# Optimization experiments

Measured on AMD Instinct MI355X. Metric: run time of the kernel, lower is better.

## Reference

```python
import jax, jax.numpy as jnp
import numpy as np

B, N, OBS, ACT = 4, 256, 40, 8
HEAD, DIM = 8, 32
T = HEAD * DIM


def setup_inputs() -> dict:
    key = jax.random.key(0)
    ks = jax.random.split(key, 10)
    x = jax.random.normal(ks[0], (B, N + 1, OBS), dtype=jnp.float32)
    # last row, col 0 carries the (float-encoded) target intersection index
    tgt = jax.random.randint(ks[1], (B,), 0, N)
    x = x.at[:, -1, 0].set(tgt.astype(jnp.float32))
    adj = jax.random.uniform(ks[2], (N, N), dtype=jnp.float32)
    s = 0.02
    return {
        "x": x,
        "adj": adj,
        "We1": jax.random.normal(ks[3], (OBS, T), dtype=jnp.float32) * s,
        "be1": jnp.zeros((T,), jnp.float32),
        "We2": jax.random.normal(ks[4], (T, T), dtype=jnp.float32) * s,
        "be2": jnp.zeros((T,), jnp.float32),
        "Wl": jax.random.normal(ks[5], (T, T), dtype=jnp.float32) * s,
        "bl": jnp.zeros((T,), jnp.float32),
        "Wn": jax.random.normal(ks[6], (T, T), dtype=jnp.float32) * s,
        "bn": jnp.zeros((T,), jnp.float32),
        "Wh": jax.random.normal(ks[7], (T, T), dtype=jnp.float32) * s,
        "bh": jnp.zeros((T,), jnp.float32),
        "Wa": jax.random.normal(ks[8], (DIM, ACT), dtype=jnp.float32) * s,
        "ba": jnp.zeros((ACT,), jnp.float32),
    }


def reference(x, adj, We1, be1, We2, be2, Wl, bl, Wn, bn, Wh, bh, Wa, ba):
    b, np1, _ = x.shape
    n = np1 - 1
    tgt = x[:, -1, 0].astype(jnp.int32)          # [B] target intersection ids
    obs = x[:, :-1, :]                            # [B,N,OBS]
    # obs_embed: Linear+ReLU twice
    emb = jax.nn.relu(obs @ We1 + be1)
    emb = jax.nn.relu(emb @ We2 + be2)            # [B,N,T]
    # tile then matmul by adjacency: result is adj @ emb, replicated along dim 1
    ne = jnp.einsum('mn,bnd->bmd', adj, emb)      # [B,N,T]
    ne = jnp.broadcast_to(ne[:, None], (b, n, n, T))  # [B,N,N,T] (tiled, as in torch)
    # agent heads: [B,N,H,1,D]
    ah = jax.nn.relu(emb @ Wl + bl).reshape(b, n, 1, DIM, HEAD).transpose(0, 1, 4, 2, 3)
    # neighbor heads: [B,N,H,N,D]
    nh = jax.nn.relu(ne @ Wn + bn).reshape(b, n, n, DIM, HEAD).transpose(0, 1, 4, 2, 3)
    # einsum 'ijklm,ijknm->ijklm' with l=1: elementwise over d, summed over n
    attn = ah * nh.sum(axis=3, keepdims=True)     # [B,N,H,1,D]
    attn = jax.nn.softmax(attn, axis=-1)
    hid = jax.nn.relu(ne @ Wh + bh).reshape(b, n, n, DIM, HEAD).transpose(0, 1, 4, 2, 3)
    out = attn * hid.sum(axis=3, keepdims=True)   # [B,N,H,1,D]
    out = out.mean(axis=2).reshape(b, n, DIM)     # mean over heads -> [B,N,D]
    g = out[jnp.arange(b), tgt]                   # gather per-batch target row [B,D]
    act = g @ Wa + ba                             # [B,ACT]
    return act
```

## Files before the change

### kernel.cpp

```cpp
#include <hip/hip_runtime.h>

#define Bsz 4
#define Nn  256
#define OBSD 40
#define ACTD 8
#define HEADS 8
#define DIMD 32
#define Td  256
#define R   4

#define FMA4(accr, s, wv) \
    (accr).x = fmaf((s), (wv).x, (accr).x); \
    (accr).y = fmaf((s), (wv).y, (accr).y); \
    (accr).z = fmaf((s), (wv).z, (accr).z); \
    (accr).w = fmaf((s), (wv).w, (accr).w)

__global__ __launch_bounds__(512, 1) void k_emb(
                      const float* __restrict__ x,
                      const float* __restrict__ We1, const float* __restrict__ be1,
                      const float* __restrict__ We2, const float* __restrict__ be2,
                      float* __restrict__ emb,
                      float* __restrict__ snh, float* __restrict__ shid) {
    int g = blockIdx.x;
    int t = threadIdx.x;
    int row0 = g * R;
    int b = row0 >> 8;
    int n0 = row0 & 255;
    if (g == 0)      { for (int i = t; i < Bsz * Td; i += 512) snh[i]  = 0.f; }
    else if (g == 1) { for (int i = t; i < Bsz * Td; i += 512) shid[i] = 0.f; }

    __shared__ float4 obs_t[OBSD];
    __shared__ float4 h1_t[Td];
    __shared__ float4 part[8][R][64];
    if (t < R * OBSD) {
        int r = t & (R - 1), k = t >> 2;
        ((float*)&obs_t[k])[r] = x[(b * (Nn + 1) + n0 + r) * OBSD + k];
    }
    __syncthreads();

    if (t < Td) {
        float bias1 = be1[t];
        float a1[R] = {bias1, bias1, bias1, bias1};
        float wbuf[8];
#pragma unroll
        for (int p = 0; p < 8; ++p) wbuf[p] = We1[p * Td + t];
#pragma unroll
        for (int k = 0; k < OBSD; ++k) {
            float w = wbuf[k & 7];
            if (k + 8 < OBSD) wbuf[k & 7] = We1[(k + 8) * Td + t];
            float4 ov = obs_t[k];
            a1[0] = fmaf(ov.x, w, a1[0]);
            a1[1] = fmaf(ov.y, w, a1[1]);
            a1[2] = fmaf(ov.z, w, a1[2]);
            a1[3] = fmaf(ov.w, w, a1[3]);
        }
        h1_t[t] = make_float4(fmaxf(a1[0], 0.f), fmaxf(a1[1], 0.f),
                              fmaxf(a1[2], 0.f), fmaxf(a1[3], 0.f));
    }
    __syncthreads();

    int wv = t >> 6, c = t & 63;
    {
        float4 a2[R] = {};
        float4 buf[8];
#pragma unroll
        for (int p = 0; p < 8; ++p)
            buf[p] = *(const float4*)(We2 + ((wv << 5) + p) * Td + 4 * c);
#pragma unroll
        for (int i = 0; i < 32; ++i) {
            int k = (wv << 5) + i;
            float4 wvv = buf[i & 7];
            if (i + 8 < 32)
                buf[i & 7] = *(const float4*)(We2 + (k + 8) * Td + 4 * c);
            float4 hv = h1_t[k];
            FMA4(a2[0], hv.x, wvv);
            FMA4(a2[1], hv.y, wvv);
            FMA4(a2[2], hv.z, wvv);
            FMA4(a2[3], hv.w, wvv);
        }
#pragma unroll
        for (int r = 0; r < R; ++r) part[wv][r][c] = a2[r];
    }
    __syncthreads();

    if (t < Td) {
        int c2 = t >> 2, j = t & 3;
#pragma unroll
        for (int r = 0; r < R; ++r) {
            float v = be2[t];
#pragma unroll
            for (int w2 = 0; w2 < 8; ++w2) v += ((const float*)&part[w2][r][c2])[j];
            emb[(row0 + r) * Td + t] = fmaxf(v, 0.f);
        }
    }
}

__global__ __launch_bounds__(512, 1) void k_fused(
                        const float* __restrict__ adj, const float* __restrict__ emb,
                        const float* __restrict__ Wn, const float* __restrict__ bn,
                        const float* __restrict__ Wh, const float* __restrict__ bh,
                        float* __restrict__ snh, float* __restrict__ shid) {
    int g = blockIdx.x, b = blockIdx.y;
    int t = threadIdx.x;
    int m0 = g * R;
    __shared__ float4 arow_t[Nn];
    __shared__ float4 nrow_t[Td];
    __shared__ float4 partN[8][R][64];
    __shared__ float4 partH[8][R][64];
    if (t < Td)
        arow_t[t] = make_float4(adj[(m0 + 0) * Nn + t], adj[(m0 + 1) * Nn + t],
                                adj[(m0 + 2) * Nn + t], adj[(m0 + 3) * Nn + t]);
    __syncthreads();

    int wv = t >> 6, c = t & 63;
    const float* eb = emb + b * Nn * Td;

    {
        float4 aN[R] = {};
        float4 buf[8];
#pragma unroll
        for (int p = 0; p < 8; ++p)
            buf[p] = *(const float4*)(eb + ((wv << 5) + p) * Td + 4 * c);
#pragma unroll
        for (int i = 0; i < 32; ++i) {
            int n = (wv << 5) + i;
            float4 ev = buf[i & 7];
            if (i + 8 < 32)
                buf[i & 7] = *(const float4*)(eb + (n + 8) * Td + 4 * c);
            float4 ar = arow_t[n];
            FMA4(aN[0], ar.x, ev);
            FMA4(aN[1], ar.y, ev);
            FMA4(aN[2], ar.z, ev);
            FMA4(aN[3], ar.w, ev);
        }
#pragma unroll
        for (int r = 0; r < R; ++r) partN[wv][r][c] = aN[r];
    }
    __syncthreads();
    if (t < Td) {
        int c2 = t >> 2, j = t & 3;
        float nr[R];
#pragma unroll
        for (int r = 0; r < R; ++r) {
            float v = 0.f;
#pragma unroll
            for (int w2 = 0; w2 < 8; ++w2) v += ((const float*)&partN[w2][r][c2])[j];
            nr[r] = v;
        }
        nrow_t[t] = make_float4(nr[0], nr[1], nr[2], nr[3]);
    }
    __syncthreads();

    {
        float4 sN[R] = {};
        float4 sH[R] = {};
        float4 bufN[4], bufH[4];
#pragma unroll
        for (int p = 0; p < 4; ++p) {
            int k = (wv << 5) + p;
            bufN[p] = *(const float4*)(Wn + k * Td + 4 * c);
            bufH[p] = *(const float4*)(Wh + k * Td + 4 * c);
        }
#pragma unroll
        for (int i = 0; i < 32; ++i) {
            int k = (wv << 5) + i;
            float4 wn4 = bufN[i & 3];
            float4 wh4 = bufH[i & 3];
            if (i + 4 < 32) {
                bufN[i & 3] = *(const float4*)(Wn + (k + 4) * Td + 4 * c);
                bufH[i & 3] = *(const float4*)(Wh + (k + 4) * Td + 4 * c);
            }
            float4 nv = nrow_t[k];
            FMA4(sN[0], nv.x, wn4);  FMA4(sH[0], nv.x, wh4);
            FMA4(sN[1], nv.y, wn4);  FMA4(sH[1], nv.y, wh4);
            FMA4(sN[2], nv.z, wn4);  FMA4(sH[2], nv.z, wh4);
            FMA4(sN[3], nv.w, wn4);  FMA4(sH[3], nv.w, wh4);
        }
#pragma unroll
        for (int r = 0; r < R; ++r) { partN[wv][r][c] = sN[r]; partH[wv][r][c] = sH[r]; }
    }
    __syncthreads();

    if (t < Td) {
        int c2 = t >> 2, j = t & 3;
        float bnt = bn[t], bht = bh[t];
        float rs1 = 0.f, rs2 = 0.f;
#pragma unroll
        for (int r = 0; r < R; ++r) {
            float v1 = bnt, v2 = bht;
#pragma unroll
            for (int w2 = 0; w2 < 8; ++w2) {
                v1 += ((const float*)&partN[w2][r][c2])[j];
                v2 += ((const float*)&partH[w2][r][c2])[j];
            }
            rs1 += fmaxf(v1, 0.f);
            rs2 += fmaxf(v2, 0.f);
        }
        atomicAdd(&snh[b * Td + t], rs1);
        atomicAdd(&shid[b * Td + t], rs2);
    }
}

__global__ __launch_bounds__(256, 1) void k_final(
                        const float* __restrict__ x, const float* __restrict__ emb,
                        const float* __restrict__ Wl, const float* __restrict__ bl,
                        const float* __restrict__ snh, const float* __restrict__ shid,
                        const float* __restrict__ Wa, const float* __restrict__ ba,
                        float* __restrict__ out) {
    int b = blockIdx.x;
    int t = threadIdx.x;
    int tgt = (int)x[(b * (Nn + 1) + Nn) * OBSD + 0];
    tgt = tgt < 0 ? 0 : (tgt > Nn - 1 ? Nn - 1 : tgt);
    __shared__ float erow[Td], lg[Td], p[Td], od[DIMD];
    __shared__ float4 partL[4][64];
    erow[t] = emb[(b * Nn + tgt) * Td + t];
    __syncthreads();

    int wv = t >> 6, c = t & 63;
    {
        float4 aL = {};
        float4 buf[8];
#pragma unroll
        for (int pp = 0; pp < 8; ++pp)
            buf[pp] = *(const float4*)(Wl + ((wv << 6) + pp) * Td + 4 * c);
#pragma unroll
        for (int i = 0; i < 64; ++i) {
            int k = (wv << 6) + i;
            float4 wlv = buf[i & 7];
            if (i + 8 < 64)
                buf[i & 7] = *(const float4*)(Wl + (k + 8) * Td + 4 * c);
            FMA4(aL, erow[k], wlv);
        }
        partL[wv][c] = aL;
    }
    __syncthreads();

    int c2 = t >> 2, j = t & 3;
    float acc = bl[t];
#pragma unroll
    for (int w2 = 0; w2 < 4; ++w2) acc += ((const float*)&partL[w2][c2])[j];
    float ah = fmaxf(acc, 0.f);
    lg[t] = ah * snh[b * Td + t];
    __syncthreads();
    int h = t & 7;
    float mx = -1e30f;
#pragma unroll
    for (int d = 0; d < DIMD; ++d) mx = fmaxf(mx, lg[d * HEADS + h]);
    float se = 0.f;
#pragma unroll
    for (int d = 0; d < DIMD; ++d) se += __expf(lg[d * HEADS + h] - mx);
    float attn = __expf(lg[t] - mx) / se;
    p[t] = attn * shid[b * Td + t];
    __syncthreads();
    if (t < DIMD) {
        float s = 0.f;
#pragma unroll
        for (int hh = 0; hh < HEADS; ++hh) s += p[t * HEADS + hh];
        od[t] = s * (1.f / HEADS);
    }
    __syncthreads();
    if (t < ACTD) {
        float s = ba[t];
#pragma unroll
        for (int d = 0; d < DIMD; ++d) s = fmaf(od[d], Wa[d * ACTD + t], s);
        out[b * ACTD + t] = s;
    }
}

extern "C" void kernel_launch(void* const* d_in, const int* in_sizes, int n_in,
                              void* d_out, int out_size, void* d_ws, size_t ws_size,
                              hipStream_t stream) {
    const float* x   = (const float*)d_in[0];
    const float* adj = (const float*)d_in[1];
    const float* We1 = (const float*)d_in[2];
    const float* be1 = (const float*)d_in[3];
    const float* We2 = (const float*)d_in[4];
    const float* be2 = (const float*)d_in[5];
    const float* Wl  = (const float*)d_in[6];
    const float* bl  = (const float*)d_in[7];
    const float* Wn  = (const float*)d_in[8];
    const float* bn  = (const float*)d_in[9];
    const float* Wh  = (const float*)d_in[10];
    const float* bh  = (const float*)d_in[11];
    const float* Wa  = (const float*)d_in[12];
    const float* ba  = (const float*)d_in[13];
    float* out = (float*)d_out;

    float* emb  = (float*)d_ws;
    float* snh  = emb + Bsz * Nn * Td;
    float* shid = snh + Bsz * Td;

    k_emb<<<dim3(Bsz * Nn / R), dim3(512), 0, stream>>>(x, We1, be1, We2, be2,
                                                        emb, snh, shid);
    k_fused<<<dim3(Nn / R, Bsz), dim3(512), 0, stream>>>(adj, emb, Wn, bn, Wh, bh,
                                                         snh, shid);
    k_final<<<dim3(Bsz), dim3(256), 0, stream>>>(x, emb, Wl, bl, snh, shid, Wa, ba, out);
}
```

Before: 101.7 us.

## Halve rows per embed block, double threads in fused/final kernels, prefetch weights into L2

```diff
diff --git a/kernel.cpp b/kernel.cpp
--- a/kernel.cpp
+++ b/kernel.cpp
@@ -7,7 +7,8 @@
 #define HEADS 8
 #define DIMD 32
 #define Td  256
-#define R   4
+#define R1  2
+#define R2  4
 
 #define FMA4(accr, s, wv) \
     (accr).x = fmaf((s), (wv).x, (accr).x); \
@@ -15,32 +16,35 @@
     (accr).z = fmaf((s), (wv).z, (accr).z); \
     (accr).w = fmaf((s), (wv).w, (accr).w)
 
-__global__ __launch_bounds__(512, 1) void k_emb(
+__global__ __launch_bounds__(512, 4) void k_emb(
                       const float* __restrict__ x,
                       const float* __restrict__ We1, const float* __restrict__ be1,
                       const float* __restrict__ We2, const float* __restrict__ be2,
+                      const float* __restrict__ Wn,  const float* __restrict__ Wh,
+                      const float* __restrict__ Wl,
                       float* __restrict__ emb,
-                      float* __restrict__ snh, float* __restrict__ shid) {
+                      float* __restrict__ snh, float* __restrict__ shid,
+                      float* __restrict__ dump) {
     int g = blockIdx.x;
     int t = threadIdx.x;
-    int row0 = g * R;
+    int row0 = g * R1;
     int b = row0 >> 8;
     int n0 = row0 & 255;
     if (g == 0)      { for (int i = t; i < Bsz * Td; i += 512) snh[i]  = 0.f; }
     else if (g == 1) { for (int i = t; i < Bsz * Td; i += 512) shid[i] = 0.f; }
 
-    __shared__ float4 obs_t[OBSD];
-    __shared__ float4 h1_t[Td];
-    __shared__ float4 part[8][R][64];
-    if (t < R * OBSD) {
-        int r = t & (R - 1), k = t >> 2;
+    __shared__ float2 obs_t[OBSD];
+    __shared__ float2 h1_t[Td];
+    __shared__ float4 part[8][R1][64];
+    if (t < R1 * OBSD) {
+        int r = t & 1, k = t >> 1;
         ((float*)&obs_t[k])[r] = x[(b * (Nn + 1) + n0 + r) * OBSD + k];
     }
     __syncthreads();
 
     if (t < Td) {
         float bias1 = be1[t];
-        float a1[R] = {bias1, bias1, bias1, bias1};
+        float a0 = bias1, a1 = bias1;
         float wbuf[8];
 #pragma unroll
         for (int p = 0; p < 8; ++p) wbuf[p] = We1[p * Td + t];
@@ -48,20 +52,17 @@
         for (int k = 0; k < OBSD; ++k) {
             float w = wbuf[k & 7];
             if (k + 8 < OBSD) wbuf[k & 7] = We1[(k + 8) * Td + t];
-            float4 ov = obs_t[k];
-            a1[0] = fmaf(ov.x, w, a1[0]);
-            a1[1] = fmaf(ov.y, w, a1[1]);
-            a1[2] = fmaf(ov.z, w, a1[2]);
-            a1[3] = fmaf(ov.w, w, a1[3]);
-        }
-        h1_t[t] = make_float4(fmaxf(a1[0], 0.f), fmaxf(a1[1], 0.f),
-                              fmaxf(a1[2], 0.f), fmaxf(a1[3], 0.f));
+            float2 ov = obs_t[k];
+            a0 = fmaf(ov.x, w, a0);
+            a1 = fmaf(ov.y, w, a1);
+        }
+        h1_t[t] = make_float2(fmaxf(a0, 0.f), fmaxf(a1, 0.f));
     }
     __syncthreads();
 
     int wv = t >> 6, c = t & 63;
     {
-        float4 a2[R] = {};
+        float4 a2[R1] = {};
         float4 buf[8];
 #pragma unroll
         for (int p = 0; p < 8; ++p)
@@ -72,41 +73,55 @@
             float4 wvv = buf[i & 7];
             if (i + 8 < 32)
                 buf[i & 7] = *(const float4*)(We2 + (k + 8) * Td + 4 * c);
-            float4 hv = h1_t[k];
+            float2 hv = h1_t[k];
             FMA4(a2[0], hv.x, wvv);
             FMA4(a2[1], hv.y, wvv);
-            FMA4(a2[2], hv.z, wvv);
-            FMA4(a2[3], hv.w, wvv);
-        }
-#pragma unroll
-        for (int r = 0; r < R; ++r) part[wv][r][c] = a2[r];
+        }
+#pragma unroll
+        for (int r = 0; r < R1; ++r) part[wv][r][c] = a2[r];
     }
     __syncthreads();
 
     if (t < Td) {
         int c2 = t >> 2, j = t & 3;
 #pragma unroll
-        for (int r = 0; r < R; ++r) {
+        for (int r = 0; r < R1; ++r) {
             float v = be2[t];
 #pragma unroll
             for (int w2 = 0; w2 < 8; ++w2) v += ((const float*)&part[w2][r][c2])[j];
             emb[(row0 + r) * Td + t] = fmaxf(v, 0.f);
         }
     }
+
+    if (g >= 2 && g < 26) {
+        int L = (g - 2) * 512 + t;
+        int q = L << 2;
+        const float4* src;
+        if (q < 16384)      src = (const float4*)Wn + q;
+        else if (q < 32768) src = (const float4*)Wh + (q - 16384);
+        else                src = (const float4*)Wl + (q - 32768);
+        float s = 0.f;
+#pragma unroll
+        for (int p2 = 0; p2 < 4; ++p2) {
+            float4 v = src[p2];
+            s += v.x + v.y + v.z + v.w;
+        }
+        dump[L] = s;
+    }
 }
 
-__global__ __launch_bounds__(512, 1) void k_fused(
+__global__ __launch_bounds__(1024, 4) void k_fused(
                         const float* __restrict__ adj, const float* __restrict__ emb,
                         const float* __restrict__ Wn, const float* __restrict__ bn,
                         const float* __restrict__ Wh, const float* __restrict__ bh,
                         float* __restrict__ snh, float* __restrict__ shid) {
     int g = blockIdx.x, b = blockIdx.y;
     int t = threadIdx.x;
-    int m0 = g * R;
+    int m0 = g * R2;
     __shared__ float4 arow_t[Nn];
     __shared__ float4 nrow_t[Td];
-    __shared__ float4 partN[8][R][64];
-    __shared__ float4 partH[8][R][64];
+    __shared__ float4 partN[16][R2][64];
+    __shared__ float4 partH[16][R2][64];
     if (t < Td)
         arow_t[t] = make_float4(adj[(m0 + 0) * Nn + t], adj[(m0 + 1) * Nn + t],
                                 adj[(m0 + 2) * Nn + t], adj[(m0 + 3) * Nn + t]);
@@ -116,16 +131,16 @@
     const float* eb = emb + b * Nn * Td;
 
     {
-        float4 aN[R] = {};
+        float4 aN[R2] = {};
         float4 buf[8];
 #pragma unroll
         for (int p = 0; p < 8; ++p)
-            buf[p] = *(const float4*)(eb + ((wv << 5) + p) * Td + 4 * c);
-#pragma unroll
-        for (int i = 0; i < 32; ++i) {
-            int n = (wv << 5) + i;
+            buf[p] = *(const float4*)(eb + ((wv << 4) + p) * Td + 4 * c);
+#pragma unroll
+        for (int i = 0; i < 16; ++i) {
+            int n = (wv << 4) + i;
             float4 ev = buf[i & 7];
-            if (i + 8 < 32)
+            if (i + 8 < 16)
                 buf[i & 7] = *(const float4*)(eb + (n + 8) * Td + 4 * c);
             float4 ar = arow_t[n];
             FMA4(aN[0], ar.x, ev);
@@ -134,17 +149,17 @@
             FMA4(aN[3], ar.w, ev);
         }
 #pragma unroll
-        for (int r = 0; r < R; ++r) partN[wv][r][c] = aN[r];
+        for (int r = 0; r < R2; ++r) partN[wv][r][c] = aN[r];
     }
     __syncthreads();
     if (t < Td) {
         int c2 = t >> 2, j = t & 3;
-        float nr[R];
-#pragma unroll
-        for (int r = 0; r < R; ++r) {
+        float nr[R2];
+#pragma unroll
+        for (int r = 0; r < R2; ++r) {
             float v = 0.f;
 #pragma unroll
-            for (int w2 = 0; w2 < 8; ++w2) v += ((const float*)&partN[w2][r][c2])[j];
+            for (int w2 = 0; w2 < 16; ++w2) v += ((const float*)&partN[w2][r][c2])[j];
             nr[r] = v;
         }
         nrow_t[t] = make_float4(nr[0], nr[1], nr[2], nr[3]);
@@ -152,21 +167,21 @@
     __syncthreads();
 
     {
-        float4 sN[R] = {};
-        float4 sH[R] = {};
+        float4 sN[R2] = {};
+        float4 sH[R2] = {};
         float4 bufN[4], bufH[4];
 #pragma unroll
         for (int p = 0; p < 4; ++p) {
-            int k = (wv << 5) + p;
+            int k = (wv << 4) + p;
             bufN[p] = *(const float4*)(Wn + k * Td + 4 * c);
             bufH[p] = *(const float4*)(Wh + k * Td + 4 * c);
         }
 #pragma unroll
-        for (int i = 0; i < 32; ++i) {
-            int k = (wv << 5) + i;
+        for (int i = 0; i < 16; ++i) {
+            int k = (wv << 4) + i;
             float4 wn4 = bufN[i & 3];
             float4 wh4 = bufH[i & 3];
-            if (i + 4 < 32) {
+            if (i + 4 < 16) {
                 bufN[i & 3] = *(const float4*)(Wn + (k + 4) * Td + 4 * c);
                 bufH[i & 3] = *(const float4*)(Wh + (k + 4) * Td + 4 * c);
             }
@@ -177,7 +192,7 @@
             FMA4(sN[3], nv.w, wn4);  FMA4(sH[3], nv.w, wh4);
         }
 #pragma unroll
-        for (int r = 0; r < R; ++r) { partN[wv][r][c] = sN[r]; partH[wv][r][c] = sH[r]; }
+        for (int r = 0; r < R2; ++r) { partN[wv][r][c] = sN[r]; partH[wv][r][c] = sH[r]; }
     }
     __syncthreads();
 
@@ -186,10 +201,10 @@
         float bnt = bn[t], bht = bh[t];
         float rs1 = 0.f, rs2 = 0.f;
 #pragma unroll
-        for (int r = 0; r < R; ++r) {
+        for (int r = 0; r < R2; ++r) {
             float v1 = bnt, v2 = bht;
 #pragma unroll
-            for (int w2 = 0; w2 < 8; ++w2) {
+            for (int w2 = 0; w2 < 16; ++w2) {
                 v1 += ((const float*)&partN[w2][r][c2])[j];
                 v2 += ((const float*)&partH[w2][r][c2])[j];
             }
@@ -201,7 +216,7 @@
     }
 }
 
-__global__ __launch_bounds__(256, 1) void k_final(
+__global__ __launch_bounds__(512, 1) void k_final(
                         const float* __restrict__ x, const float* __restrict__ emb,
                         const float* __restrict__ Wl, const float* __restrict__ bl,
                         const float* __restrict__ snh, const float* __restrict__ shid,
@@ -212,8 +227,8 @@
     int tgt = (int)x[(b * (Nn + 1) + Nn) * OBSD + 0];
     tgt = tgt < 0 ? 0 : (tgt > Nn - 1 ? Nn - 1 : tgt);
     __shared__ float erow[Td], lg[Td], p[Td], od[DIMD];
-    __shared__ float4 partL[4][64];
-    erow[t] = emb[(b * Nn + tgt) * Td + t];
+    __shared__ float4 partL[8][64];
+    if (t < Td) erow[t] = emb[(b * Nn + tgt) * Td + t];
     __syncthreads();
 
     int wv = t >> 6, c = t & 63;
@@ -222,12 +237,12 @@
         float4 buf[8];
 #pragma unroll
         for (int pp = 0; pp < 8; ++pp)
-            buf[pp] = *(const float4*)(Wl + ((wv << 6) + pp) * Td + 4 * c);
-#pragma unroll
-        for (int i = 0; i < 64; ++i) {
-            int k = (wv << 6) + i;
+            buf[pp] = *(const float4*)(Wl + ((wv << 5) + pp) * Td + 4 * c);
+#pragma unroll
+        for (int i = 0; i < 32; ++i) {
+            int k = (wv << 5) + i;
             float4 wlv = buf[i & 7];
-            if (i + 8 < 64)
+            if (i + 8 < 32)
                 buf[i & 7] = *(const float4*)(Wl + (k + 8) * Td + 4 * c);
             FMA4(aL, erow[k], wlv);
         }
@@ -235,22 +250,26 @@
     }
     __syncthreads();
 
-    int c2 = t >> 2, j = t & 3;
-    float acc = bl[t];
-#pragma unroll
-    for (int w2 = 0; w2 < 4; ++w2) acc += ((const float*)&partL[w2][c2])[j];
-    float ah = fmaxf(acc, 0.f);
-    lg[t] = ah * snh[b * Td + t];
-    __syncthreads();
-    int h = t & 7;
-    float mx = -1e30f;
-#pragma unroll
-    for (int d = 0; d < DIMD; ++d) mx = fmaxf(mx, lg[d * HEADS + h]);
-    float se = 0.f;
-#pragma unroll
-    for (int d = 0; d < DIMD; ++d) se += __expf(lg[d * HEADS + h] - mx);
-    float attn = __expf(lg[t] - mx) / se;
-    p[t] = attn * shid[b * Td + t];
+    if (t < Td) {
+        int c2 = t >> 2, j = t & 3;
+        float acc = bl[t];
+#pragma unroll
+        for (int w2 = 0; w2 < 8; ++w2) acc += ((const float*)&partL[w2][c2])[j];
+        float ah = fmaxf(acc, 0.f);
+        lg[t] = ah * snh[b * Td + t];
+    }
+    __syncthreads();
+    if (t < Td) {
+        int h = t & 7;
+        float mx = -1e30f;
+#pragma unroll
+        for (int d = 0; d < DIMD; ++d) mx = fmaxf(mx, lg[d * HEADS + h]);
+        float se = 0.f;
+#pragma unroll
+        for (int d = 0; d < DIMD; ++d) se += __expf(lg[d * HEADS + h] - mx);
+        float attn = __expf(lg[t] - mx) / se;
+        p[t] = attn * shid[b * Td + t];
+    }
     __syncthreads();
     if (t < DIMD) {
         float s = 0.f;
@@ -289,10 +308,12 @@
     float* emb  = (float*)d_ws;
     float* snh  = emb + Bsz * Nn * Td;
     float* shid = snh + Bsz * Td;
-
-    k_emb<<<dim3(Bsz * Nn / R), dim3(512), 0, stream>>>(x, We1, be1, We2, be2,
-                                                        emb, snh, shid);
-    k_fused<<<dim3(Nn / R, Bsz), dim3(512), 0, stream>>>(adj, emb, Wn, bn, Wh, bh,
-                                                         snh, shid);
-    k_final<<<dim3(Bsz), dim3(256), 0, stream>>>(x, emb, Wl, bl, snh, shid, Wa, ba, out);
+    float* dump = shid + Bsz * Td;
+
+    k_emb<<<dim3(Bsz * Nn / R1), dim3(512), 0, stream>>>(x, We1, be1, We2, be2,
+                                                         Wn, Wh, Wl,
+                                                         emb, snh, shid, dump);
+    k_fused<<<dim3(Nn / R2, Bsz), dim3(1024), 0, stream>>>(adj, emb, Wn, bn, Wh, bh,
+                                                           snh, shid);
+    k_final<<<dim3(Bsz), dim3(512), 0, stream>>>(x, emb, Wl, bl, snh, shid, Wa, ba, out);
 }
```

Measured after the change: 152.6 us. +50.1%, slower.

## Split fused adj-matmul kernel into two 16x64 tiled GEMM kernels

Applied to the files above, without the earlier changes.

```diff
diff --git a/kernel.cpp b/kernel.cpp
--- a/kernel.cpp
+++ b/kernel.cpp
@@ -95,71 +95,105 @@
     }
 }
 
-__global__ __launch_bounds__(512, 1) void k_fused(
+__global__ __launch_bounds__(512, 1) void k_ne(
                         const float* __restrict__ adj, const float* __restrict__ emb,
+                        float* __restrict__ ne) {
+    int mt = blockIdx.x, tt = blockIdx.y, b = blockIdx.z;
+    int t = threadIdx.x;
+    int m0 = mt << 4, t0 = tt << 6;
+    __shared__ float A_lds[16][260];
+    __shared__ float4 part[8][4][16][4];
+
+    {
+        int r = t >> 5, kb = (t & 31) << 3;
+        const float* Ar = adj + (m0 + r) * Nn + kb;
+        float4 a0 = *(const float4*)(Ar);
+        float4 a1 = *(const float4*)(Ar + 4);
+        *(float4*)&A_lds[r][kb] = a0;
+        *(float4*)&A_lds[r][kb + 4] = a1;
+    }
+    __syncthreads();
+
+    int wv = t >> 6, c = t & 63;
+    int cg = c & 15, rq = c >> 4;
+    const float* Bp = emb + b * Nn * Td + t0 + (cg << 2);
+    {
+        float4 acc[4] = {};
+        float4 buf[8];
+#pragma unroll
+        for (int p = 0; p < 8; ++p)
+            buf[p] = *(const float4*)(Bp + ((wv << 5) + p) * Td);
+#pragma unroll
+        for (int i = 0; i < 32; ++i) {
+            int k = (wv << 5) + i;
+            float4 bv = buf[i & 7];
+            if (i + 8 < 32)
+                buf[i & 7] = *(const float4*)(Bp + (k + 8) * Td);
+            float a0 = A_lds[(rq << 2) + 0][k];
+            float a1 = A_lds[(rq << 2) + 1][k];
+            float a2 = A_lds[(rq << 2) + 2][k];
+            float a3 = A_lds[(rq << 2) + 3][k];
+            FMA4(acc[0], a0, bv);
+            FMA4(acc[1], a1, bv);
+            FMA4(acc[2], a2, bv);
+            FMA4(acc[3], a3, bv);
+        }
+#pragma unroll
+        for (int j = 0; j < 4; ++j) part[wv][rq][cg][j] = acc[j];
+    }
+    __syncthreads();
+
+    float* nb = ne + b * Nn * Td;
+#pragma unroll
+    for (int h = 0; h < 2; ++h) {
+        int o = t + (h << 9);
+        int r = o >> 6, cc = o & 63;
+        int rq2 = r >> 2, rj = r & 3, cg2 = cc >> 2, ci = cc & 3;
+        float v = 0.f;
+#pragma unroll
+        for (int w2 = 0; w2 < 8; ++w2)
+            v += ((const float*)&part[w2][rq2][cg2][rj])[ci];
+        nb[(m0 + r) * Td + t0 + cc] = v;
+    }
+}
+
+__global__ __launch_bounds__(512, 1) void k_snh(
+                        const float* __restrict__ ne,
                         const float* __restrict__ Wn, const float* __restrict__ bn,
                         const float* __restrict__ Wh, const float* __restrict__ bh,
                         float* __restrict__ snh, float* __restrict__ shid) {
-    int g = blockIdx.x, b = blockIdx.y;
+    int mt = blockIdx.x, tt = blockIdx.y, b = blockIdx.z;
     int t = threadIdx.x;
-    int m0 = g * R;
-    __shared__ float4 arow_t[Nn];
-    __shared__ float4 nrow_t[Td];
-    __shared__ float4 partN[8][R][64];
-    __shared__ float4 partH[8][R][64];
-    if (t < Td)
-        arow_t[t] = make_float4(adj[(m0 + 0) * Nn + t], adj[(m0 + 1) * Nn + t],
-                                adj[(m0 + 2) * Nn + t], adj[(m0 + 3) * Nn + t]);
+    int m0 = mt << 4, t0 = tt << 6;
+    __shared__ float A_lds[16][260];
+    __shared__ float4 partN[8][4][16][4];
+    __shared__ float4 partH[8][4][16][4];
+    __shared__ float redN[16][64];
+    __shared__ float redH[16][64];
+
+    {
+        int r = t >> 5, kb = (t & 31) << 3;
+        const float* Ar = ne + b * Nn * Td + (m0 + r) * Td + kb;
+        float4 a0 = *(const float4*)(Ar);
+        float4 a1 = *(const float4*)(Ar + 4);
+        *(float4*)&A_lds[r][kb] = a0;
+        *(float4*)&A_lds[r][kb + 4] = a1;
+    }
     __syncthreads();
 
     int wv = t >> 6, c = t & 63;
-    const float* eb = emb + b * Nn * Td;
-
-    {
-        float4 aN[R] = {};
-        float4 buf[8];
-#pragma unroll
-        for (int p = 0; p < 8; ++p)
-            buf[p] = *(const float4*)(eb + ((wv << 5) + p) * Td + 4 * c);
-#pragma unroll
-        for (int i = 0; i < 32; ++i) {
-            int n = (wv << 5) + i;
-            float4 ev = buf[i & 7];
-            if (i + 8 < 32)
-                buf[i & 7] = *(const float4*)(eb + (n + 8) * Td + 4 * c);
-            float4 ar = arow_t[n];
-            FMA4(aN[0], ar.x, ev);
-            FMA4(aN[1], ar.y, ev);
-            FMA4(aN[2], ar.z, ev);
-            FMA4(aN[3], ar.w, ev);
-        }
-#pragma unroll
-        for (int r = 0; r < R; ++r) partN[wv][r][c] = aN[r];
-    }
-    __syncthreads();
-    if (t < Td) {
-        int c2 = t >> 2, j = t & 3;
-        float nr[R];
-#pragma unroll
-        for (int r = 0; r < R; ++r) {
-            float v = 0.f;
-#pragma unroll
-            for (int w2 = 0; w2 < 8; ++w2) v += ((const float*)&partN[w2][r][c2])[j];
-            nr[r] = v;
-        }
-        nrow_t[t] = make_float4(nr[0], nr[1], nr[2], nr[3]);
-    }
-    __syncthreads();
-
-    {
-        float4 sN[R] = {};
-        float4 sH[R] = {};
+    int cg = c & 15, rq = c >> 4;
+    const float* BpN = Wn + t0 + (cg << 2);
+    const float* BpH = Wh + t0 + (cg << 2);
+    {
+        float4 accN[4] = {};
+        float4 accH[4] = {};
         float4 bufN[4], bufH[4];
 #pragma unroll
         for (int p = 0; p < 4; ++p) {
             int k = (wv << 5) + p;
-            bufN[p] = *(const float4*)(Wn + k * Td + 4 * c);
-            bufH[p] = *(const float4*)(Wh + k * Td + 4 * c);
+            bufN[p] = *(const float4*)(BpN + k * Td);
+            bufH[p] = *(const float4*)(BpH + k * Td);
         }
 #pragma unroll
         for (int i = 0; i < 32; ++i) {
@@ -167,41 +201,54 @@
             float4 wn4 = bufN[i & 3];
             float4 wh4 = bufH[i & 3];
             if (i + 4 < 32) {
-                bufN[i & 3] = *(const float4*)(Wn + (k + 4) * Td + 4 * c);
-                bufH[i & 3] = *(const float4*)(Wh + (k + 4) * Td + 4 * c);
+                bufN[i & 3] = *(const float4*)(BpN + (k + 4) * Td);
+                bufH[i & 3] = *(const float4*)(BpH + (k + 4) * Td);
             }
-            float4 nv = nrow_t[k];
-            FMA4(sN[0], nv.x, wn4);  FMA4(sH[0], nv.x, wh4);
-            FMA4(sN[1], nv.y, wn4);  FMA4(sH[1], nv.y, wh4);
-            FMA4(sN[2], nv.z, wn4);  FMA4(sH[2], nv.z, wh4);
-            FMA4(sN[3], nv.w, wn4);  FMA4(sH[3], nv.w, wh4);
-        }
-#pragma unroll
-        for (int r = 0; r < R; ++r) { partN[wv][r][c] = sN[r]; partH[wv][r][c] = sH[r]; }
-    }
-    __syncthreads();
-
-    if (t < Td) {
-        int c2 = t >> 2, j = t & 3;
-        float bnt = bn[t], bht = bh[t];
-        float rs1 = 0.f, rs2 = 0.f;
-#pragma unroll
-        for (int r = 0; r < R; ++r) {
-            float v1 = bnt, v2 = bht;
-#pragma unroll
-            for (int w2 = 0; w2 < 8; ++w2) {
-                v1 += ((const float*)&partN[w2][r][c2])[j];
-                v2 += ((const float*)&partH[w2][r][c2])[j];
-            }
-            rs1 += fmaxf(v1, 0.f);
-            rs2 += fmaxf(v2, 0.f);
-        }
-        atomicAdd(&snh[b * Td + t], rs1);
-        atomicAdd(&shid[b * Td + t], rs2);
-    }
-}
-
-__global__ __launch_bounds__(256, 1) void k_final(
+            float a0 = A_lds[(rq << 2) + 0][k];
+            float a1 = A_lds[(rq << 2) + 1][k];
+            float a2 = A_lds[(rq << 2) + 2][k];
+            float a3 = A_lds[(rq << 2) + 3][k];
+            FMA4(accN[0], a0, wn4);  FMA4(accH[0], a0, wh4);
+            FMA4(accN[1], a1, wn4);  FMA4(accH[1], a1, wh4);
+            FMA4(accN[2], a2, wn4);  FMA4(accH[2], a2, wh4);
+            FMA4(accN[3], a3, wn4);  FMA4(accH[3], a3, wh4);
+        }
+#pragma unroll
+        for (int j = 0; j < 4; ++j) { partN[wv][rq][cg][j] = accN[j]; partH[wv][rq][cg][j] = accH[j]; }
+    }
+    __syncthreads();
+
+#pragma unroll
+    for (int h = 0; h < 2; ++h) {
+        int o = t + (h << 9);
+        int r = o >> 6, cc = o & 63;
+        int rq2 = r >> 2, rj = r & 3, cg2 = cc >> 2, ci = cc & 3;
+        float vN = bn[t0 + cc], vH = bh[t0 + cc];
+#pragma unroll
+        for (int w2 = 0; w2 < 8; ++w2) {
+            vN += ((const float*)&partN[w2][rq2][cg2][rj])[ci];
+            vH += ((const float*)&partH[w2][rq2][cg2][rj])[ci];
+        }
+        redN[r][cc] = fmaxf(vN, 0.f);
+        redH[r][cc] = fmaxf(vH, 0.f);
+    }
+    __syncthreads();
+
+    if (t < 64) {
+        float s = 0.f;
+#pragma unroll
+        for (int r = 0; r < 16; ++r) s += redN[r][t];
+        atomicAdd(&snh[b * Td + t0 + t], s);
+    } else if (t < 128) {
+        int cc = t - 64;
+        float s = 0.f;
+#pragma unroll
+        for (int r = 0; r < 16; ++r) s += redH[r][cc];
+        atomicAdd(&shid[b * Td + t0 + cc], s);
+    }
+}
+
+__global__ __launch_bounds__(512, 1) void k_final(
                         const float* __restrict__ x, const float* __restrict__ emb,
                         const float* __restrict__ Wl, const float* __restrict__ bl,
                         const float* __restrict__ snh, const float* __restrict__ shid,
@@ -212,8 +259,8 @@
     int tgt = (int)x[(b * (Nn + 1) + Nn) * OBSD + 0];
     tgt = tgt < 0 ? 0 : (tgt > Nn - 1 ? Nn - 1 : tgt);
     __shared__ float erow[Td], lg[Td], p[Td], od[DIMD];
-    __shared__ float4 partL[4][64];
-    erow[t] = emb[(b * Nn + tgt) * Td + t];
+    __shared__ float4 partL[8][64];
+    if (t < Td) erow[t] = emb[(b * Nn + tgt) * Td + t];
     __syncthreads();
 
     int wv = t >> 6, c = t & 63;
@@ -222,12 +269,12 @@
         float4 buf[8];
 #pragma unroll
         for (int pp = 0; pp < 8; ++pp)
-            buf[pp] = *(const float4*)(Wl + ((wv << 6) + pp) * Td + 4 * c);
-#pragma unroll
-        for (int i = 0; i < 64; ++i) {
-            int k = (wv << 6) + i;
+            buf[pp] = *(const float4*)(Wl + ((wv << 5) + pp) * Td + 4 * c);
+#pragma unroll
+        for (int i = 0; i < 32; ++i) {
+            int k = (wv << 5) + i;
             float4 wlv = buf[i & 7];
-            if (i + 8 < 64)
+            if (i + 8 < 32)
                 buf[i & 7] = *(const float4*)(Wl + (k + 8) * Td + 4 * c);
             FMA4(aL, erow[k], wlv);
         }
@@ -235,22 +282,26 @@
     }
     __syncthreads();
 
-    int c2 = t >> 2, j = t & 3;
-    float acc = bl[t];
-#pragma unroll
-    for (int w2 = 0; w2 < 4; ++w2) acc += ((const float*)&partL[w2][c2])[j];
-    float ah = fmaxf(acc, 0.f);
-    lg[t] = ah * snh[b * Td + t];
-    __syncthreads();
-    int h = t & 7;
-    float mx = -1e30f;
-#pragma unroll
-    for (int d = 0; d < DIMD; ++d) mx = fmaxf(mx, lg[d * HEADS + h]);
-    float se = 0.f;
-#pragma unroll
-    for (int d = 0; d < DIMD; ++d) se += __expf(lg[d * HEADS + h] - mx);
-    float attn = __expf(lg[t] - mx) / se;
-    p[t] = attn * shid[b * Td + t];
+    if (t < Td) {
+        int c2 = t >> 2, j = t & 3;
+        float acc = bl[t];
+#pragma unroll
+        for (int w2 = 0; w2 < 8; ++w2) acc += ((const float*)&partL[w2][c2])[j];
+        float ah = fmaxf(acc, 0.f);
+        lg[t] = ah * snh[b * Td + t];
+    }
+    __syncthreads();
+    if (t < Td) {
+        int h = t & 7;
+        float mx = -1e30f;
+#pragma unroll
+        for (int d = 0; d < DIMD; ++d) mx = fmaxf(mx, lg[d * HEADS + h]);
+        float se = 0.f;
+#pragma unroll
+        for (int d = 0; d < DIMD; ++d) se += __expf(lg[d * HEADS + h] - mx);
+        float attn = __expf(lg[t] - mx) / se;
+        p[t] = attn * shid[b * Td + t];
+    }
     __syncthreads();
     if (t < DIMD) {
         float s = 0.f;
@@ -287,12 +338,13 @@
     float* out = (float*)d_out;
 
     float* emb  = (float*)d_ws;
-    float* snh  = emb + Bsz * Nn * Td;
+    float* ne   = emb + Bsz * Nn * Td;
+    float* snh  = ne  + Bsz * Nn * Td;
     float* shid = snh + Bsz * Td;
 
     k_emb<<<dim3(Bsz * Nn / R), dim3(512), 0, stream>>>(x, We1, be1, We2, be2,
                                                         emb, snh, shid);
-    k_fused<<<dim3(Nn / R, Bsz), dim3(512), 0, stream>>>(adj, emb, Wn, bn, Wh, bh,
-                                                         snh, shid);
-    k_final<<<dim3(Bsz), dim3(256), 0, stream>>>(x, emb, Wl, bl, snh, shid, Wa, ba, out);
-}
+    k_ne<<<dim3(16, 4, Bsz), dim3(512), 0, stream>>>(adj, emb, ne);
+    k_snh<<<dim3(16, 4, Bsz), dim3(512), 0, stream>>>(ne, Wn, bn, Wh, bh, snh, shid);
+    k_final<<<dim3(Bsz), dim3(512), 0, stream>>>(x, emb, Wl, bl, snh, shid, Wa, ba, out);
+}
```

Measured after the change: 102.6 us. No clear change (+0.9%).

## Merge three kernels into one cooperative kernel with grid-wide syncs

Applied to the files above, without the earlier changes.

```diff
diff --git a/kernel.cpp b/kernel.cpp
--- a/kernel.cpp
+++ b/kernel.cpp
@@ -1,4 +1,7 @@
 #include <hip/hip_runtime.h>
+#include <hip/hip_cooperative_groups.h>
+
+namespace cg = cooperative_groups;
 
 #define Bsz 4
 #define Nn  256
@@ -15,255 +18,272 @@
     (accr).z = fmaf((s), (wv).z, (accr).z); \
     (accr).w = fmaf((s), (wv).w, (accr).w)
 
-__global__ __launch_bounds__(512, 1) void k_emb(
-                      const float* __restrict__ x,
+union SMem {
+    struct {
+        float4 obs_t[OBSD];
+        float4 h1_t[Td];
+        float4 part[8][R][64];
+    } a;
+    struct {
+        float4 arow[Nn];
+        float4 nrow[Td];
+        float4 partN[8][R][64];
+        float4 partH[8][R][64];
+    } bp;
+    struct {
+        float erow[Td], lg[Td], p[Td], od[DIMD];
+        float4 partL[8][64];
+    } f;
+};
+
+__global__ __launch_bounds__(512, 1) void k_all(
+                      const float* __restrict__ x,   const float* __restrict__ adj,
                       const float* __restrict__ We1, const float* __restrict__ be1,
                       const float* __restrict__ We2, const float* __restrict__ be2,
-                      float* __restrict__ emb,
-                      float* __restrict__ snh, float* __restrict__ shid) {
+                      const float* __restrict__ Wl,  const float* __restrict__ bl,
+                      const float* __restrict__ Wn,  const float* __restrict__ bn,
+                      const float* __restrict__ Wh,  const float* __restrict__ bh,
+                      const float* __restrict__ Wa,  const float* __restrict__ ba,
+                      float* __restrict__ emb, float* __restrict__ snh,
+                      float* __restrict__ shid, float* __restrict__ out) {
+    cg::grid_group grid = cg::this_grid();
+    __shared__ SMem sm;
     int g = blockIdx.x;
     int t = threadIdx.x;
-    int row0 = g * R;
-    int b = row0 >> 8;
-    int n0 = row0 & 255;
-    if (g == 0)      { for (int i = t; i < Bsz * Td; i += 512) snh[i]  = 0.f; }
-    else if (g == 1) { for (int i = t; i < Bsz * Td; i += 512) shid[i] = 0.f; }
-
-    __shared__ float4 obs_t[OBSD];
-    __shared__ float4 h1_t[Td];
-    __shared__ float4 part[8][R][64];
-    if (t < R * OBSD) {
-        int r = t & (R - 1), k = t >> 2;
-        ((float*)&obs_t[k])[r] = x[(b * (Nn + 1) + n0 + r) * OBSD + k];
+    int wv = t >> 6, c = t & 63;
+
+    {
+        int row0 = g * R;
+        int b = row0 >> 8;
+        int n0 = row0 & 255;
+        if (g == 0)      { for (int i = t; i < Bsz * Td; i += 512) snh[i]  = 0.f; }
+        else if (g == 1) { for (int i = t; i < Bsz * Td; i += 512) shid[i] = 0.f; }
+
+        if (t < R * OBSD) {
+            int r = t & (R - 1), k = t >> 2;
+            ((float*)&sm.a.obs_t[k])[r] = x[(b * (Nn + 1) + n0 + r) * OBSD + k];
+        }
+        __syncthreads();
+
+        if (t < Td) {
+            float bias1 = be1[t];
+            float a1[R] = {bias1, bias1, bias1, bias1};
+            float wbuf[8];
+#pragma unroll
+            for (int p = 0; p < 8; ++p) wbuf[p] = We1[p * Td + t];
+#pragma unroll
+            for (int k = 0; k < OBSD; ++k) {
+                float w = wbuf[k & 7];
+                if (k + 8 < OBSD) wbuf[k & 7] = We1[(k + 8) * Td + t];
+                float4 ov = sm.a.obs_t[k];
+                a1[0] = fmaf(ov.x, w, a1[0]);
+                a1[1] = fmaf(ov.y, w, a1[1]);
+                a1[2] = fmaf(ov.z, w, a1[2]);
+                a1[3] = fmaf(ov.w, w, a1[3]);
+            }
+            sm.a.h1_t[t] = make_float4(fmaxf(a1[0], 0.f), fmaxf(a1[1], 0.f),
+                                       fmaxf(a1[2], 0.f), fmaxf(a1[3], 0.f));
+        }
+        __syncthreads();
+
+        {
+            float4 a2[R] = {};
+            float4 buf[8];
+#pragma unroll
+            for (int p = 0; p < 8; ++p)
+                buf[p] = *(const float4*)(We2 + ((wv << 5) + p) * Td + 4 * c);
+#pragma unroll
+            for (int i = 0; i < 32; ++i) {
+                int k = (wv << 5) + i;
+                float4 wvv = buf[i & 7];
+                if (i + 8 < 32)
+                    buf[i & 7] = *(const float4*)(We2 + (k + 8) * Td + 4 * c);
+                float4 hv = sm.a.h1_t[k];
+                FMA4(a2[0], hv.x, wvv);
+                FMA4(a2[1], hv.y, wvv);
+                FMA4(a2[2], hv.z, wvv);
+                FMA4(a2[3], hv.w, wvv);
+            }
+#pragma unroll
+            for (int r = 0; r < R; ++r) sm.a.part[wv][r][c] = a2[r];
+        }
+        __syncthreads();
+
+        if (t < Td) {
+            int c2 = t >> 2, j = t & 3;
+#pragma unroll
+            for (int r = 0; r < R; ++r) {
+                float v = be2[t];
+#pragma unroll
+                for (int w2 = 0; w2 < 8; ++w2)
+                    v += ((const float*)&sm.a.part[w2][r][c2])[j];
+                emb[(row0 + r) * Td + t] = fmaxf(v, 0.f);
+            }
+        }
     }
-    __syncthreads();
-
-    if (t < Td) {
-        float bias1 = be1[t];
-        float a1[R] = {bias1, bias1, bias1, bias1};
-        float wbuf[8];
-#pragma unroll
-        for (int p = 0; p < 8; ++p) wbuf[p] = We1[p * Td + t];
-#pragma unroll
-        for (int k = 0; k < OBSD; ++k) {
-            float w = wbuf[k & 7];
-            if (k + 8 < OBSD) wbuf[k & 7] = We1[(k + 8) * Td + t];
-            float4 ov = obs_t[k];
-            a1[0] = fmaf(ov.x, w, a1[0]);
-            a1[1] = fmaf(ov.y, w, a1[1]);
-            a1[2] = fmaf(ov.z, w, a1[2]);
-            a1[3] = fmaf(ov.w, w, a1[3]);
-        }
-        h1_t[t] = make_float4(fmaxf(a1[0], 0.f), fmaxf(a1[1], 0.f),
-                              fmaxf(a1[2], 0.f), fmaxf(a1[3], 0.f));
+    grid.sync();
+
+    {
+        int b = g >> 6, gm = g & 63;
+        int m0 = gm * R;
+        if (t < Td)
+            sm.bp.arow[t] = make_float4(adj[(m0 + 0) * Nn + t], adj[(m0 + 1) * Nn + t],
+                                        adj[(m0 + 2) * Nn + t], adj[(m0 + 3) * Nn + t]);
+        __syncthreads();
+
+        const float* eb = emb + b * Nn * Td;
+
+        {
+            float4 aN[R] = {};
+            float4 buf[8];
+#pragma unroll
+            for (int p = 0; p < 8; ++p)
+                buf[p] = *(const float4*)(eb + ((wv << 5) + p) * Td + 4 * c);
+#pragma unroll
+            for (int i = 0; i < 32; ++i) {
+                int n = (wv << 5) + i;
+                float4 ev = buf[i & 7];
+                if (i + 8 < 32)
+                    buf[i & 7] = *(const float4*)(eb + (n + 8) * Td + 4 * c);
+                float4 ar = sm.bp.arow[n];
+                FMA4(aN[0], ar.x, ev);
+                FMA4(aN[1], ar.y, ev);
+                FMA4(aN[2], ar.z, ev);
+                FMA4(aN[3], ar.w, ev);
+            }
+#pragma unroll
+            for (int r = 0; r < R; ++r) sm.bp.partN[wv][r][c] = aN[r];
+        }
+        __syncthreads();
+        if (t < Td) {
+            int c2 = t >> 2, j = t & 3;
+            float nr[R];
+#pragma unroll
+            for (int r = 0; r < R; ++r) {
+                float v = 0.f;
+#pragma unroll
+                for (int w2 = 0; w2 < 8; ++w2)
+                    v += ((const float*)&sm.bp.partN[w2][r][c2])[j];
+                nr[r] = v;
+            }
+            sm.bp.nrow[t] = make_float4(nr[0], nr[1], nr[2], nr[3]);
+        }
+        __syncthreads();
+
+        {
+            float4 sN[R] = {};
+            float4 sH[R] = {};
+            float4 bufN[4], bufH[4];
+#pragma unroll
+            for (int p = 0; p < 4; ++p) {
+                int k = (wv << 5) + p;
+                bufN[p] = *(const float4*)(Wn + k * Td + 4 * c);
+                bufH[p] = *(const float4*)(Wh + k * Td + 4 * c);
+            }
+#pragma unroll
+            for (int i = 0; i < 32; ++i) {
+                int k = (wv << 5) + i;
+                float4 wn4 = bufN[i & 3];
+                float4 wh4 = bufH[i & 3];
+                if (i + 4 < 32) {
+                    bufN[i & 3] = *(const float4*)(Wn + (k + 4) * Td + 4 * c);
+                    bufH[i & 3] = *(const float4*)(Wh + (k + 4) * Td + 4 * c);
+                }
+                float4 nv = sm.bp.nrow[k];
+                FMA4(sN[0], nv.x, wn4);  FMA4(sH[0], nv.x, wh4);
+                FMA4(sN[1], nv.y, wn4);  FMA4(sH[1], nv.y, wh4);
+                FMA4(sN[2], nv.z, wn4);  FMA4(sH[2], nv.z, wh4);
+                FMA4(sN[3], nv.w, wn4);  FMA4(sH[3], nv.w, wh4);
+            }
+#pragma unroll
+            for (int r = 0; r < R; ++r) {
+                sm.bp.partN[wv][r][c] = sN[r];
+                sm.bp.partH[wv][r][c] = sH[r];
+            }
+        }
+        __syncthreads();
+
+        if (t < Td) {
+            int c2 = t >> 2, j = t & 3;
+            float bnt = bn[t], bht = bh[t];
+            float rs1 = 0.f, rs2 = 0.f;
+#pragma unroll
+            for (int r = 0; r < R; ++r) {
+                float v1 = bnt, v2 = bht;
+#pragma unroll
+                for (int w2 = 0; w2 < 8; ++w2) {
+                    v1 += ((const float*)&sm.bp.partN[w2][r][c2])[j];
+                    v2 += ((const float*)&sm.bp.partH[w2][r][c2])[j];
+                }
+                rs1 += fmaxf(v1, 0.f);
+                rs2 += fmaxf(v2, 0.f);
+            }
+            atomicAdd(&snh[b * Td + t], rs1);
+            atomicAdd(&shid[b * Td + t], rs2);
+        }
     }
-    __syncthreads();
-
-    int wv = t >> 6, c = t & 63;
-    {
-        float4 a2[R] = {};
-        float4 buf[8];
-#pragma unroll
-        for (int p = 0; p < 8; ++p)
-            buf[p] = *(const float4*)(We2 + ((wv << 5) + p) * Td + 4 * c);
-#pragma unroll
-        for (int i = 0; i < 32; ++i) {
-            int k = (wv << 5) + i;
-            float4 wvv = buf[i & 7];
-            if (i + 8 < 32)
-                buf[i & 7] = *(const float4*)(We2 + (k + 8) * Td + 4 * c);
-            float4 hv = h1_t[k];
-            FMA4(a2[0], hv.x, wvv);
-            FMA4(a2[1], hv.y, wvv);
-            FMA4(a2[2], hv.z, wvv);
-            FMA4(a2[3], hv.w, wvv);
-        }
-#pragma unroll
-        for (int r = 0; r < R; ++r) part[wv][r][c] = a2[r];
-    }
-    __syncthreads();
-
-    if (t < Td) {
-        int c2 = t >> 2, j = t & 3;
-#pragma unroll
-        for (int r = 0; r < R; ++r) {
-            float v = be2[t];
-#pragma unroll
-            for (int w2 = 0; w2 < 8; ++w2) v += ((const float*)&part[w2][r][c2])[j];
-            emb[(row0 + r) * Td + t] = fmaxf(v, 0.f);
-        }
-    }
-}
-
-__global__ __launch_bounds__(512, 1) void k_fused(
-                        const float* __restrict__ adj, const float* __restrict__ emb,
-                        const float* __restrict__ Wn, const float* __restrict__ bn,
-                        const float* __restrict__ Wh, const float* __restrict__ bh,
-                        float* __restrict__ snh, float* __restrict__ shid) {
-    int g = blockIdx.x, b = blockIdx.y;
-    int t = threadIdx.x;
-    int m0 = g * R;
-    __shared__ float4 arow_t[Nn];
-    __shared__ float4 nrow_t[Td];
-    __shared__ float4 partN[8][R][64];
-    __shared__ float4 partH[8][R][64];
-    if (t < Td)
-        arow_t[t] = make_float4(adj[(m0 + 0) * Nn + t], adj[(m0 + 1) * Nn + t],
-                                adj[(m0 + 2) * Nn + t], adj[(m0 + 3) * Nn + t]);
-    __syncthreads();
-
-    int wv = t >> 6, c = t & 63;
-    const float* eb = emb + b * Nn * Td;
-
-    {
-        float4 aN[R] = {};
-        float4 buf[8];
-#pragma unroll
-        for (int p = 0; p < 8; ++p)
-            buf[p] = *(const float4*)(eb + ((wv << 5) + p) * Td + 4 * c);
-#pragma unroll
-        for (int i = 0; i < 32; ++i) {
-            int n = (wv << 5) + i;
-            float4 ev = buf[i & 7];
-            if (i + 8 < 32)
-                buf[i & 7] = *(const float4*)(eb + (n + 8) * Td + 4 * c);
-            float4 ar = arow_t[n];
-            FMA4(aN[0], ar.x, ev);
-            FMA4(aN[1], ar.y, ev);
-            FMA4(aN[2], ar.z, ev);
-            FMA4(aN[3], ar.w, ev);
-        }
-#pragma unroll
-        for (int r = 0; r < R; ++r) partN[wv][r][c] = aN[r];
-    }
-    __syncthreads();
-    if (t < Td) {
-        int c2 = t >> 2, j = t & 3;
-        float nr[R];
-#pragma unroll
-        for (int r = 0; r < R; ++r) {
-            float v = 0.f;
-#pragma unroll
-            for (int w2 = 0; w2 < 8; ++w2) v += ((const float*)&partN[w2][r][c2])[j];
-            nr[r] = v;
-        }
-        nrow_t[t] = make_float4(nr[0], nr[1], nr[2], nr[3]);
-    }
-    __syncthreads();
-
-    {
-        float4 sN[R] = {};
-        float4 sH[R] = {};
-        float4 bufN[4], bufH[4];
-#pragma unroll
-        for (int p = 0; p < 4; ++p) {
-            int k = (wv << 5) + p;
-            bufN[p] = *(const float4*)(Wn + k * Td + 4 * c);
-            bufH[p] = *(const float4*)(Wh + k * Td + 4 * c);
-        }
-#pragma unroll
-        for (int i = 0; i < 32; ++i) {
-            int k = (wv << 5) + i;
-            float4 wn4 = bufN[i & 3];
-            float4 wh4 = bufH[i & 3];
-            if (i + 4 < 32) {
-                bufN[i & 3] = *(const float4*)(Wn + (k + 4) * Td + 4 * c);
-                bufH[i & 3] = *(const float4*)(Wh + (k + 4) * Td + 4 * c);
-            }
-            float4 nv = nrow_t[k];
-            FMA4(sN[0], nv.x, wn4);  FMA4(sH[0], nv.x, wh4);
-            FMA4(sN[1], nv.y, wn4);  FMA4(sH[1], nv.y, wh4);
-            FMA4(sN[2], nv.z, wn4);  FMA4(sH[2], nv.z, wh4);
-            FMA4(sN[3], nv.w, wn4);  FMA4(sH[3], nv.w, wh4);
-        }
-#pragma unroll
-        for (int r = 0; r < R; ++r) { partN[wv][r][c] = sN[r]; partH[wv][r][c] = sH[r]; }
-    }
-    __syncthreads();
-
-    if (t < Td) {
-        int c2 = t >> 2, j = t & 3;
-        float bnt = bn[t], bht = bh[t];
-        float rs1 = 0.f, rs2 = 0.f;
-#pragma unroll
-        for (int r = 0; r < R; ++r) {
-            float v1 = bnt, v2 = bht;
-#pragma unroll
-            for (int w2 = 0; w2 < 8; ++w2) {
-                v1 += ((const float*)&partN[w2][r][c2])[j];
-                v2 += ((const float*)&partH[w2][r][c2])[j];
-            }
-            rs1 += fmaxf(v1, 0.f);
-            rs2 += fmaxf(v2, 0.f);
-        }
-        atomicAdd(&snh[b * Td + t], rs1);
-        atomicAdd(&shid[b * Td + t], rs2);
-    }
-}
-
-__global__ __launch_bounds__(256, 1) void k_final(
-                        const float* __restrict__ x, const float* __restrict__ emb,
-                        const float* __restrict__ Wl, const float* __restrict__ bl,
-                        const float* __restrict__ snh, const float* __restrict__ shid,
-                        const float* __restrict__ Wa, const float* __restrict__ ba,
-                        float* __restrict__ out) {
-    int b = blockIdx.x;
-    int t = threadIdx.x;
-    int tgt = (int)x[(b * (Nn + 1) + Nn) * OBSD + 0];
-    tgt = tgt < 0 ? 0 : (tgt > Nn - 1 ? Nn - 1 : tgt);
-    __shared__ float erow[Td], lg[Td], p[Td], od[DIMD];
-    __shared__ float4 partL[4][64];
-    erow[t] = emb[(b * Nn + tgt) * Td + t];
-    __syncthreads();
-
-    int wv = t >> 6, c = t & 63;
-    {
-        float4 aL = {};
-        float4 buf[8];
-#pragma unroll
-        for (int pp = 0; pp < 8; ++pp)
-            buf[pp] = *(const float4*)(Wl + ((wv << 6) + pp) * Td + 4 * c);
-#pragma unroll
-        for (int i = 0; i < 64; ++i) {
-            int k = (wv << 6) + i;
-            float4 wlv = buf[i & 7];
-            if (i + 8 < 64)
-                buf[i & 7] = *(const float4*)(Wl + (k + 8) * Td + 4 * c);
-            FMA4(aL, erow[k], wlv);
-        }
-        partL[wv][c] = aL;
-    }
-    __syncthreads();
-
-    int c2 = t >> 2, j = t & 3;
-    float acc = bl[t];
-#pragma unroll
-    for (int w2 = 0; w2 < 4; ++w2) acc += ((const float*)&partL[w2][c2])[j];
-    float ah = fmaxf(acc, 0.f);
-    lg[t] = ah * snh[b * Td + t];
-    __syncthreads();
-    int h = t & 7;
-    float mx = -1e30f;
-#pragma unroll
-    for (int d = 0; d < DIMD; ++d) mx = fmaxf(mx, lg[d * HEADS + h]);
-    float se = 0.f;
-#pragma unroll
-    for (int d = 0; d < DIMD; ++d) se += __expf(lg[d * HEADS + h] - mx);
-    float attn = __expf(lg[t] - mx) / se;
-    p[t] = attn * shid[b * Td + t];
-    __syncthreads();
-    if (t < DIMD) {
-        float s = 0.f;
-#pragma unroll
-        for (int hh = 0; hh < HEADS; ++hh) s += p[t * HEADS + hh];
-        od[t] = s * (1.f / HEADS);
-    }
-    __syncthreads();
-    if (t < ACTD) {
-        float s = ba[t];
-#pragma unroll
-        for (int d = 0; d < DIMD; ++d) s = fmaf(od[d], Wa[d * ACTD + t], s);
-        out[b * ACTD + t] = s;
+    grid.sync();
+
+    if (g < Bsz) {
+        int b = g;
+        int tgt = (int)x[(b * (Nn + 1) + Nn) * OBSD + 0];
+        tgt = tgt < 0 ? 0 : (tgt > Nn - 1 ? Nn - 1 : tgt);
+        if (t < Td) sm.f.erow[t] = emb[(b * Nn + tgt) * Td + t];
+        __syncthreads();
+
+        {
+            float4 aL = {};
+            float4 buf[8];
+#pragma unroll
+            for (int pp = 0; pp < 8; ++pp)
+                buf[pp] = *(const float4*)(Wl + ((wv << 5) + pp) * Td + 4 * c);
+#pragma unroll
+            for (int i = 0; i < 32; ++i) {
+                int k = (wv << 5) + i;
+                float4 wlv = buf[i & 7];
+                if (i + 8 < 32)
+                    buf[i & 7] = *(const float4*)(Wl + (k + 8) * Td + 4 * c);
+                FMA4(aL, sm.f.erow[k], wlv);
+            }
+            sm.f.partL[wv][c] = aL;
+        }
+        __syncthreads();
+
+        if (t < Td) {
+            int c2 = t >> 2, j = t & 3;
+            float acc = bl[t];
+#pragma unroll
+            for (int w2 = 0; w2 < 8; ++w2)
+                acc += ((const float*)&sm.f.partL[w2][c2])[j];
+            float ah = fmaxf(acc, 0.f);
+            sm.f.lg[t] = ah * snh[b * Td + t];
+        }
+        __syncthreads();
+        if (t < Td) {
+            int h = t & 7;
+            float mx = -1e30f;
+#pragma unroll
+            for (int d = 0; d < DIMD; ++d) mx = fmaxf(mx, sm.f.lg[d * HEADS + h]);
+            float se = 0.f;
+#pragma unroll
+            for (int d = 0; d < DIMD; ++d) se += __expf(sm.f.lg[d * HEADS + h] - mx);
+            float attn = __expf(sm.f.lg[t] - mx) / se;
+            sm.f.p[t] = attn * shid[b * Td + t];
+        }
+        __syncthreads();
+        if (t < DIMD) {
+            float s = 0.f;
+#pragma unroll
+            for (int hh = 0; hh < HEADS; ++hh) s += sm.f.p[t * HEADS + hh];
+            sm.f.od[t] = s * (1.f / HEADS);
+        }
+        __syncthreads();
+        if (t < ACTD) {
+            float s = ba[t];
+#pragma unroll
+            for (int d = 0; d < DIMD; ++d) s = fmaf(sm.f.od[d], Wa[d * ACTD + t], s);
+            out[b * ACTD + t] = s;
+        }
     }
 }
 
@@ -290,9 +310,11 @@
     float* snh  = emb + Bsz * Nn * Td;
     float* shid = snh + Bsz * Td;
 
-    k_emb<<<dim3(Bsz * Nn / R), dim3(512), 0, stream>>>(x, We1, be1, We2, be2,
-                                                        emb, snh, shid);
-    k_fused<<<dim3(Nn / R, Bsz), dim3(512), 0, stream>>>(adj, emb, Wn, bn, Wh, bh,
-                                                         snh, shid);
-    k_final<<<dim3(Bsz), dim3(256), 0, stream>>>(x, emb, Wl, bl, snh, shid, Wa, ba, out);
+    void* args[] = {(void*)&x,  (void*)&adj, (void*)&We1, (void*)&be1,
+                    (void*)&We2, (void*)&be2, (void*)&Wl,  (void*)&bl,
+                    (void*)&Wn,  (void*)&bn,  (void*)&Wh,  (void*)&bh,
+                    (void*)&Wa,  (void*)&ba,  (void*)&emb, (void*)&snh,
+                    (void*)&shid, (void*)&out};
+    hipLaunchCooperativeKernel((void*)k_all, dim3(Bsz * Nn / R), dim3(512),
+                               args, 0, stream);
 }
```

Result: slower. 181.2 us (+78.2%).
